# Optimization experiments

Measured on AMD Instinct MI355X. Metric: run time of the kernel, lower is better.

Reference implementation:

```python
import jax, jax.numpy as jnp
import numpy as np

N_N = 100000
N_E = 1600000
IN_DIM = 128
OUT_DIM = 128


def setup_inputs() -> dict:
    key = jax.random.key(0)
    k1, k2, k3, k4 = jax.random.split(key, 4)
    feats_n = jax.random.normal(k1, (N_N, IN_DIM), dtype=jnp.float32)
    # hs: guarantee every node appears at least once as a row (head) so degree > 0,
    # matching well-posed inputs for D**(-1/2) in the original module.
    hs = jnp.concatenate([
        jnp.arange(N_N, dtype=jnp.int64),
        jax.random.randint(k2, (N_E - N_N,), 0, N_N, dtype=jnp.int64),
    ])
    ts = jax.random.randint(k3, (N_E,), 0, N_N, dtype=jnp.int64)
    edges = jnp.stack([hs, ts], axis=0)  # [2, N_e]
    # Linear weight: normal(0,1) scaled by 1/sqrt(out_dim), no bias.
    weight = jax.random.normal(k4, (OUT_DIM, IN_DIM), dtype=jnp.float32) / np.sqrt(OUT_DIM)
    return {"feats_n": feats_n, "edges": edges, "weight": weight}


def reference(feats_n, edges, weight):
    hs, ts = edges[0], edges[1]
    n = feats_n.shape[0]
    # Degree = row-sum of adjacency (rows indexed by hs)
    deg = jax.ops.segment_sum(jnp.ones_like(hs, dtype=feats_n.dtype), hs, num_segments=n)
    sqrt_d_inv = deg ** (-0.5)  # [N_n]
    scaled = sqrt_d_inv[:, None] * feats_n  # [N_n, d]
    # SpMM: out[h] = sum over edges (h, t) of scaled[t]
    agg = jax.ops.segment_sum(scaled[ts], hs, num_segments=n)  # [N_n, d]
    msg = sqrt_d_inv[:, None] * agg
    out = msg @ weight.T  # Linear, no bias
    return jax.nn.relu(out)
```

## Files before the change

kernel.cpp:

```cpp
#include <hip/hip_runtime.h>

#define IN_DIM 128
#define CAP 64
#define NODE_SHIFT 8
#define BIN_NODES 256
#define NB_MAX 512
#define BCAP 5120
#define BINCAP_E 10240
#define CHUNK 4096

typedef __attribute__((ext_vector_type(8))) short bf16x8;
typedef __attribute__((ext_vector_type(4))) float f32x4;
typedef __attribute__((ext_vector_type(2))) float f32x2;

__device__ __forceinline__ unsigned short f2bf(float f) {
    unsigned int u = __float_as_uint(f);
    u += 0x7FFFu + ((u >> 16) & 1u);
    return (unsigned short)(u >> 16);
}

__global__ void k_prep(const float* __restrict__ W, bf16x8* __restrict__ Wsw,
                       int* __restrict__ bincur, int nbins,
                       unsigned int* __restrict__ dummy, float* __restrict__ rsd,
                       int n_n) {
    int gi = blockIdx.x * 256 + threadIdx.x;
    if (gi < nbins) bincur[gi] = 0;
    if (gi < 64) dummy[gi] = 0;
    if (gi == 64) rsd[n_n] = 0.0f;
    if (gi >= 2048) return;
    int n = gi >> 4, g = gi & 15;
    const float* wp = W + n * IN_DIM + g * 8;
    float4 a = *(const float4*)wp;
    float4 b = *(const float4*)(wp + 4);
    bf16x8 v;
    v[0] = (short)f2bf(a.x); v[1] = (short)f2bf(a.y);
    v[2] = (short)f2bf(a.z); v[3] = (short)f2bf(a.w);
    v[4] = (short)f2bf(b.x); v[5] = (short)f2bf(b.y);
    v[6] = (short)f2bf(b.z); v[7] = (short)f2bf(b.w);
    Wsw[n * 16 + (g ^ (n & 7))] = v;
}

__global__ __launch_bounds__(256) void k_partition(const int* __restrict__ edges, int n_e,
                                                   int nbins,
                                                   unsigned int* __restrict__ pairs,
                                                   int* __restrict__ bincur) {
    __shared__ unsigned long long sp[CHUNK];
    __shared__ int hist[NB_MAX];
    __shared__ int base[NB_MAX];
    int tid = threadIdx.x;
    int e0 = blockIdx.x * CHUNK;
    int nloc = n_e - e0;
    if (nloc > CHUNK) nloc = CHUNK;
    for (int i = tid; i < nbins; i += 256) hist[i] = 0;
    __syncthreads();
    for (int i = tid; i < nloc; i += 256) {
        int h = edges[e0 + i];
        int t = edges[n_e + e0 + i];
        sp[i] = ((unsigned long long)(unsigned int)h << 17) | (unsigned int)t;
        atomicAdd(&hist[h >> NODE_SHIFT], 1);
    }
    __syncthreads();
    for (int b = tid; b < nbins; b += 256) {
        int c = hist[b];
        base[b] = c ? atomicAdd(&bincur[b], c) : 0;
        hist[b] = 0;
    }
    __syncthreads();
    for (int i = tid; i < nloc; i += 256) {
        unsigned long long p = sp[i];
        int b = (int)(p >> (17 + NODE_SHIFT));
        int pos = atomicAdd(&hist[b], 1);
        int g = base[b] + pos;
        if (g < BCAP) pairs[(size_t)b * BCAP + g] = (unsigned int)(p & 0x1FFFFFFu);
    }
}

__global__ __launch_bounds__(256) void k_binmfma(const unsigned int* __restrict__ pairs,
                                                 const int* __restrict__ bincur,
                                                 int* __restrict__ bucket,
                                                 int2* __restrict__ rowinfo,
                                                 float* __restrict__ rsd,
                                                 const float* __restrict__ X,
                                                 const bf16x8* __restrict__ Wg,
                                                 unsigned short* __restrict__ Y2,
                                                 int n_n, int nbins) {
    __shared__ union {
        struct {
            unsigned int sp[BCAP];
            int lcur[BIN_NODES];
            int sbase[BIN_NODES];
            int wsum[4];
        } bs;
        bf16x8 wl[2048];
    } u;
    int tid = threadIdx.x;

    if ((int)blockIdx.x < nbins) {
        int b = blockIdx.x;
        u.bs.lcur[tid] = 0;
        __syncthreads();
        int n = bincur[b];
        if (n > BCAP) n = BCAP;
        const unsigned int* pp = pairs + (size_t)b * BCAP;
        for (int i = tid; i < n; i += 256) {
            unsigned int p = pp[i];
            u.bs.sp[i] = p;
            atomicAdd(&u.bs.lcur[p >> 17], 1);
        }
        __syncthreads();
        int draw = u.bs.lcur[tid];
        int dcap = draw < CAP ? draw : CAP;
        int v = (dcap + 15) & ~15;
        int lane = tid & 63, w = tid >> 6;
        int x = v;
        #pragma unroll
        for (int off = 1; off < 64; off <<= 1) {
            int y = __shfl_up(x, off);
            if (lane >= off) x += y;
        }
        if (lane == 63) u.bs.wsum[w] = x;
        __syncthreads();
        int wo = 0;
        for (int k = 0; k < w; ++k) wo += u.bs.wsum[k];
        int mybase = wo + x - v;
        u.bs.sbase[tid] = mybase;
        u.bs.lcur[tid] = 0;
        __syncthreads();
        int gbase = b * BINCAP_E;
        for (int i = tid; i < n; i += 256) {
            unsigned int p = u.bs.sp[i];
            int li = p >> 17;
            int t = p & 0x1FFFF;
            int pos = atomicAdd(&u.bs.lcur[li], 1);
            if (pos < CAP) {
                int idx = u.bs.sbase[li] + pos;
                if (idx < BINCAP_E) bucket[gbase + idx] = t;
            }
        }
        __syncthreads();
        int h = (b << NODE_SHIFT) + tid;
        if (h < n_n) {
            for (int s = dcap; s < v; ++s) {
                int idx = mybase + s;
                if (idx < BINCAP_E) bucket[gbase + idx] = n_n;
            }
            rowinfo[h] = make_int2(gbase + mybase, dcap);
            rsd[h] = draw > 0 ? rsqrtf((float)draw) : 0.0f;
        }
    } else {
        int M = n_n;
        int mb = blockIdx.x - nbins;
        for (int i = tid; i < 2048; i += 256) u.wl[i] = Wg[i];
        __syncthreads();
        int slab = mb * 4 + (tid >> 6);
        int m0 = slab * 16;
        if (m0 >= M) return;
        int l = tid & 63;
        int lm = l & 15, lk = l >> 4;
        int row = m0 + lm;
        int rowc = row < M ? row : M - 1;
        bf16x8 xf[4];
        const float* xbase = X + (size_t)rowc * IN_DIM + lk * 8;
        #pragma unroll
        for (int ks = 0; ks < 4; ++ks) {
            float4 a = *(const float4*)(xbase + ks * 32);
            float4 b2 = *(const float4*)(xbase + ks * 32 + 4);
            bf16x8 v;
            v[0] = (short)f2bf(a.x); v[1] = (short)f2bf(a.y);
            v[2] = (short)f2bf(a.z); v[3] = (short)f2bf(a.w);
            v[4] = (short)f2bf(b2.x); v[5] = (short)f2bf(b2.y);
            v[6] = (short)f2bf(b2.z); v[7] = (short)f2bf(b2.w);
            xf[ks] = v;
        }
        #pragma unroll
        for (int nt = 0; nt < 8; ++nt) {
            f32x4 acc = {0.f, 0.f, 0.f, 0.f};
            #pragma unroll
            for (int ks = 0; ks < 4; ++ks) {
                int nn = nt * 16 + lm;
                int g = ks * 4 + lk;
                bf16x8 wf = u.wl[nn * 16 + (g ^ (nn & 7))];
                acc = __builtin_amdgcn_mfma_f32_16x16x32_bf16(wf, xf[ks], acc, 0, 0, 0);
            }
            if (row < M) {
                unsigned int lo = (unsigned int)f2bf(acc[0]) |
                                  ((unsigned int)f2bf(acc[1]) << 16);
                unsigned int hi = (unsigned int)f2bf(acc[2]) |
                                  ((unsigned int)f2bf(acc[3]) << 16);
                uint2* yp = (uint2*)(Y2 + (size_t)row * IN_DIM + nt * 16 + lk * 4);
                *yp = make_uint2(lo, hi);
            }
        }
    }
}

__global__ __launch_bounds__(256) void k_agg(const uint4* __restrict__ Y4,
                                             const int* __restrict__ bucket,
                                             const int2* __restrict__ rowinfo,
                                             const float* __restrict__ rsd,
                                             float* __restrict__ out, int n_n) {
    int gw = (int)((blockIdx.x * 256u + threadIdx.x) >> 6);
    int lane = threadIdx.x & 63;
    if (gw >= n_n) return;
    int2 ri = rowinfo[gw];
    int d = ri.y;
    int nb = (d + 15) >> 4;
    const uint4* bk4 = (const uint4*)(bucket + ri.x);
    int grp = lane >> 4, a = lane & 15;
    f32x2 a0 = {0.f, 0.f}, a1 = {0.f, 0.f}, a2 = {0.f, 0.f}, a3 = {0.f, 0.f};

    uint4 tv = bk4[grp];
    for (int b = 0; b < nb; ++b) {
        int bn = (b + 1 < nb) ? b + 1 : b;
        uint4 tvn = bk4[bn * 4 + grp];
        float s0 = rsd[tv.x], s1 = rsd[tv.y], s2 = rsd[tv.z], s3 = rsd[tv.w];
        uint4 v0 = Y4[(size_t)tv.x * 16 + a];
        uint4 v1 = Y4[(size_t)tv.y * 16 + a];
        uint4 v2 = Y4[(size_t)tv.z * 16 + a];
        uint4 v3 = Y4[(size_t)tv.w * 16 + a];
        #define ACCUM(V, S)                                                   \
        {                                                                     \
            f32x2 sv; sv[0] = (S); sv[1] = (S);                               \
            f32x2 x;                                                          \
            x[0] = __uint_as_float((V).x << 16);                              \
            x[1] = __uint_as_float((V).x & 0xffff0000u);                      \
            asm("v_pk_fma_f32 %0, %1, %2, %0" : "+v"(a0) : "v"(x), "v"(sv));  \
            x[0] = __uint_as_float((V).y << 16);                              \
            x[1] = __uint_as_float((V).y & 0xffff0000u);                      \
            asm("v_pk_fma_f32 %0, %1, %2, %0" : "+v"(a1) : "v"(x), "v"(sv));  \
            x[0] = __uint_as_float((V).z << 16);                              \
            x[1] = __uint_as_float((V).z & 0xffff0000u);                      \
            asm("v_pk_fma_f32 %0, %1, %2, %0" : "+v"(a2) : "v"(x), "v"(sv));  \
            x[0] = __uint_as_float((V).w << 16);                              \
            x[1] = __uint_as_float((V).w & 0xffff0000u);                      \
            asm("v_pk_fma_f32 %0, %1, %2, %0" : "+v"(a3) : "v"(x), "v"(sv));  \
        }
        ACCUM(v0, s0) ACCUM(v1, s1) ACCUM(v2, s2) ACCUM(v3, s3)
        #undef ACCUM
        tv = tvn;
    }
    #define MERGE(A)                                                          \
    {                                                                         \
        A[0] += __shfl_xor(A[0], 16); A[1] += __shfl_xor(A[1], 16);           \
        A[0] += __shfl_xor(A[0], 32); A[1] += __shfl_xor(A[1], 32);           \
    }
    MERGE(a0) MERGE(a1) MERGE(a2) MERGE(a3)
    #undef MERGE
    if (lane < 16) {
        float s = rsd[gw];
        float4 o0 = make_float4(fmaxf(a0[0] * s, 0.f), fmaxf(a0[1] * s, 0.f),
                                fmaxf(a1[0] * s, 0.f), fmaxf(a1[1] * s, 0.f));
        float4 o1 = make_float4(fmaxf(a2[0] * s, 0.f), fmaxf(a2[1] * s, 0.f),
                                fmaxf(a3[0] * s, 0.f), fmaxf(a3[1] * s, 0.f));
        float4* op = (float4*)(out + (size_t)gw * IN_DIM + a * 8);
        op[0] = o0;
        op[1] = o1;
    }
}

extern "C" void kernel_launch(void* const* d_in, const int* in_sizes, int n_in,
                              void* d_out, int out_size, void* d_ws, size_t ws_size,
                              hipStream_t stream) {
    const float* X = (const float*)d_in[0];
    const int* edges = (const int*)d_in[1];
    const float* W = (const float*)d_in[2];
    int n_n = in_sizes[0] / IN_DIM;
    int n_e = in_sizes[1] / 2;
    int nbins = (n_n + BIN_NODES - 1) >> NODE_SHIFT;

    char* ws = (char*)d_ws;
    size_t o = 0;
    auto take = [&](size_t bytes) -> char* {
        char* p = ws + o;
        o += (bytes + 511) & ~(size_t)511;
        return p;
    };
    float* rsd = (float*)take((size_t)(n_n + 1) * 4);
    int2* rowinfo = (int2*)take((size_t)n_n * 8);
    int* bucket = (int*)take((size_t)nbins * BINCAP_E * 4);
    unsigned short* Y2 = (unsigned short*)take((size_t)(n_n + 1) * IN_DIM * 2);
    unsigned int* pairs = (unsigned int*)take((size_t)nbins * BCAP * 4);
    int* bincur = (int*)take((size_t)nbins * 4);
    bf16x8* Wsw = (bf16x8*)take(2048 * 16);

    int nslab = (n_n + 15) / 16;
    int nmf = (nslab + 3) / 4;
    k_prep<<<8, 256, 0, stream>>>(W, Wsw, bincur, nbins,
                                  (unsigned int*)(Y2 + (size_t)n_n * IN_DIM), rsd, n_n);
    k_partition<<<(n_e + CHUNK - 1) / CHUNK, 256, 0, stream>>>(edges, n_e, nbins, pairs, bincur);
    k_binmfma<<<nbins + nmf, 256, 0, stream>>>(pairs, bincur, bucket, rowinfo, rsd,
                                               X, Wsw, Y2, n_n, nbins);
    k_agg<<<(n_n + 3) / 4, 256, 0, stream>>>((const uint4*)Y2, bucket, rowinfo, rsd,
                                             (float*)d_out, n_n);
}
```

Before: 119.2 us.

## Co-schedule dense GEMM with edge partition instead of bin scatter

Moves the X·W^T bf16 MFMA blocks out of the bin-scatter kernel and into the edge-partition kernel, which is then split into a fused partition+GEMM launch and a standalone bin-scatter launch. The dense GEMM now overlaps the atomic-heavy edge partition, while the bin-scatter runs alone afterward. This rebalances work across kernels, but the partition blocks now share an LDS union sized for the larger 32KB sp array, which may reduce occupancy of the GEMM blocks.

```diff
diff --git a/kernel.cpp b/kernel.cpp
--- a/kernel.cpp
+++ b/kernel.cpp
@@ -40,116 +40,53 @@
     Wsw[n * 16 + (g ^ (n & 7))] = v;
 }
 
-__global__ __launch_bounds__(256) void k_partition(const int* __restrict__ edges, int n_e,
-                                                   int nbins,
-                                                   unsigned int* __restrict__ pairs,
-                                                   int* __restrict__ bincur) {
-    __shared__ unsigned long long sp[CHUNK];
-    __shared__ int hist[NB_MAX];
-    __shared__ int base[NB_MAX];
-    int tid = threadIdx.x;
-    int e0 = blockIdx.x * CHUNK;
-    int nloc = n_e - e0;
-    if (nloc > CHUNK) nloc = CHUNK;
-    for (int i = tid; i < nbins; i += 256) hist[i] = 0;
-    __syncthreads();
-    for (int i = tid; i < nloc; i += 256) {
-        int h = edges[e0 + i];
-        int t = edges[n_e + e0 + i];
-        sp[i] = ((unsigned long long)(unsigned int)h << 17) | (unsigned int)t;
-        atomicAdd(&hist[h >> NODE_SHIFT], 1);
-    }
-    __syncthreads();
-    for (int b = tid; b < nbins; b += 256) {
-        int c = hist[b];
-        base[b] = c ? atomicAdd(&bincur[b], c) : 0;
-        hist[b] = 0;
-    }
-    __syncthreads();
-    for (int i = tid; i < nloc; i += 256) {
-        unsigned long long p = sp[i];
-        int b = (int)(p >> (17 + NODE_SHIFT));
-        int pos = atomicAdd(&hist[b], 1);
-        int g = base[b] + pos;
-        if (g < BCAP) pairs[(size_t)b * BCAP + g] = (unsigned int)(p & 0x1FFFFFFu);
-    }
-}
-
-__global__ __launch_bounds__(256) void k_binmfma(const unsigned int* __restrict__ pairs,
-                                                 const int* __restrict__ bincur,
-                                                 int* __restrict__ bucket,
-                                                 int2* __restrict__ rowinfo,
-                                                 float* __restrict__ rsd,
-                                                 const float* __restrict__ X,
-                                                 const bf16x8* __restrict__ Wg,
-                                                 unsigned short* __restrict__ Y2,
-                                                 int n_n, int nbins) {
+__global__ __launch_bounds__(256) void k_partgemm(const int* __restrict__ edges, int n_e,
+                                                  int nbins, int npart,
+                                                  unsigned int* __restrict__ pairs,
+                                                  int* __restrict__ bincur,
+                                                  const float* __restrict__ X,
+                                                  const bf16x8* __restrict__ Wg,
+                                                  unsigned short* __restrict__ Y2,
+                                                  int n_n) {
     __shared__ union {
         struct {
-            unsigned int sp[BCAP];
-            int lcur[BIN_NODES];
-            int sbase[BIN_NODES];
-            int wsum[4];
-        } bs;
+            unsigned long long sp[CHUNK];
+            int hist[NB_MAX];
+            int base[NB_MAX];
+        } pt;
         bf16x8 wl[2048];
     } u;
     int tid = threadIdx.x;
 
-    if ((int)blockIdx.x < nbins) {
-        int b = blockIdx.x;
-        u.bs.lcur[tid] = 0;
-        __syncthreads();
-        int n = bincur[b];
-        if (n > BCAP) n = BCAP;
-        const unsigned int* pp = pairs + (size_t)b * BCAP;
-        for (int i = tid; i < n; i += 256) {
-            unsigned int p = pp[i];
-            u.bs.sp[i] = p;
-            atomicAdd(&u.bs.lcur[p >> 17], 1);
-        }
-        __syncthreads();
-        int draw = u.bs.lcur[tid];
-        int dcap = draw < CAP ? draw : CAP;
-        int v = (dcap + 15) & ~15;
-        int lane = tid & 63, w = tid >> 6;
-        int x = v;
-        #pragma unroll
-        for (int off = 1; off < 64; off <<= 1) {
-            int y = __shfl_up(x, off);
-            if (lane >= off) x += y;
-        }
-        if (lane == 63) u.bs.wsum[w] = x;
-        __syncthreads();
-        int wo = 0;
-        for (int k = 0; k < w; ++k) wo += u.bs.wsum[k];
-        int mybase = wo + x - v;
-        u.bs.sbase[tid] = mybase;
-        u.bs.lcur[tid] = 0;
-        __syncthreads();
-        int gbase = b * BINCAP_E;
-        for (int i = tid; i < n; i += 256) {
-            unsigned int p = u.bs.sp[i];
-            int li = p >> 17;
-            int t = p & 0x1FFFF;
-            int pos = atomicAdd(&u.bs.lcur[li], 1);
-            if (pos < CAP) {
-                int idx = u.bs.sbase[li] + pos;
-                if (idx < BINCAP_E) bucket[gbase + idx] = t;
-            }
-        }
-        __syncthreads();
-        int h = (b << NODE_SHIFT) + tid;
-        if (h < n_n) {
-            for (int s = dcap; s < v; ++s) {
-                int idx = mybase + s;
-                if (idx < BINCAP_E) bucket[gbase + idx] = n_n;
-            }
-            rowinfo[h] = make_int2(gbase + mybase, dcap);
-            rsd[h] = draw > 0 ? rsqrtf((float)draw) : 0.0f;
+    if ((int)blockIdx.x < npart) {
+        int e0 = blockIdx.x * CHUNK;
+        int nloc = n_e - e0;
+        if (nloc > CHUNK) nloc = CHUNK;
+        for (int i = tid; i < nbins; i += 256) u.pt.hist[i] = 0;
+        __syncthreads();
+        for (int i = tid; i < nloc; i += 256) {
+            int h = edges[e0 + i];
+            int t = edges[n_e + e0 + i];
+            u.pt.sp[i] = ((unsigned long long)(unsigned int)h << 17) | (unsigned int)t;
+            atomicAdd(&u.pt.hist[h >> NODE_SHIFT], 1);
+        }
+        __syncthreads();
+        for (int b = tid; b < nbins; b += 256) {
+            int c = u.pt.hist[b];
+            u.pt.base[b] = c ? atomicAdd(&bincur[b], c) : 0;
+            u.pt.hist[b] = 0;
+        }
+        __syncthreads();
+        for (int i = tid; i < nloc; i += 256) {
+            unsigned long long p = u.pt.sp[i];
+            int b = (int)(p >> (17 + NODE_SHIFT));
+            int pos = atomicAdd(&u.pt.hist[b], 1);
+            int g = u.pt.base[b] + pos;
+            if (g < BCAP) pairs[(size_t)b * BCAP + g] = (unsigned int)(p & 0x1FFFFFFu);
         }
     } else {
         int M = n_n;
-        int mb = blockIdx.x - nbins;
+        int mb = blockIdx.x - npart;
         for (int i = tid; i < 2048; i += 256) u.wl[i] = Wg[i];
         __syncthreads();
         int slab = mb * 4 + (tid >> 6);
@@ -191,6 +128,69 @@
                 *yp = make_uint2(lo, hi);
             }
         }
+    }
+}
+
+__global__ __launch_bounds__(256) void k_binscatter(const unsigned int* __restrict__ pairs,
+                                                    const int* __restrict__ bincur,
+                                                    int* __restrict__ bucket,
+                                                    int2* __restrict__ rowinfo,
+                                                    float* __restrict__ rsd, int n_n) {
+    __shared__ unsigned int sp[BCAP];
+    __shared__ int lcur[BIN_NODES];
+    __shared__ int sbase[BIN_NODES];
+    __shared__ int wsum[4];
+    int b = blockIdx.x;
+    int tid = threadIdx.x;
+    lcur[tid] = 0;
+    __syncthreads();
+    int n = bincur[b];
+    if (n > BCAP) n = BCAP;
+    const unsigned int* pp = pairs + (size_t)b * BCAP;
+    for (int i = tid; i < n; i += 256) {
+        unsigned int p = pp[i];
+        sp[i] = p;
+        atomicAdd(&lcur[p >> 17], 1);
+    }
+    __syncthreads();
+    int draw = lcur[tid];
+    int dcap = draw < CAP ? draw : CAP;
+    int v = (dcap + 15) & ~15;
+    int lane = tid & 63, w = tid >> 6;
+    int x = v;
+    #pragma unroll
+    for (int off = 1; off < 64; off <<= 1) {
+        int y = __shfl_up(x, off);
+        if (lane >= off) x += y;
+    }
+    if (lane == 63) wsum[w] = x;
+    __syncthreads();
+    int wo = 0;
+    for (int k = 0; k < w; ++k) wo += wsum[k];
+    int mybase = wo + x - v;
+    sbase[tid] = mybase;
+    lcur[tid] = 0;
+    __syncthreads();
+    int gbase = b * BINCAP_E;
+    for (int i = tid; i < n; i += 256) {
+        unsigned int p = sp[i];
+        int li = p >> 17;
+        int t = p & 0x1FFFF;
+        int pos = atomicAdd(&lcur[li], 1);
+        if (pos < CAP) {
+            int idx = sbase[li] + pos;
+            if (idx < BINCAP_E) bucket[gbase + idx] = t;
+        }
+    }
+    __syncthreads();
+    int h = (b << NODE_SHIFT) + tid;
+    if (h < n_n) {
+        for (int s = dcap; s < v; ++s) {
+            int idx = mybase + s;
+            if (idx < BINCAP_E) bucket[gbase + idx] = n_n;
+        }
+        rowinfo[h] = make_int2(gbase + mybase, dcap);
+        rsd[h] = draw > 0 ? rsqrtf((float)draw) : 0.0f;
     }
 }
 
@@ -285,11 +285,12 @@
 
     int nslab = (n_n + 15) / 16;
     int nmf = (nslab + 3) / 4;
+    int npart = (n_e + CHUNK - 1) / CHUNK;
     k_prep<<<8, 256, 0, stream>>>(W, Wsw, bincur, nbins,
                                   (unsigned int*)(Y2 + (size_t)n_n * IN_DIM), rsd, n_n);
-    k_partition<<<(n_e + CHUNK - 1) / CHUNK, 256, 0, stream>>>(edges, n_e, nbins, pairs, bincur);
-    k_binmfma<<<nbins + nmf, 256, 0, stream>>>(pairs, bincur, bucket, rowinfo, rsd,
-                                               X, Wsw, Y2, n_n, nbins);
+    k_partgemm<<<npart + nmf, 256, 0, stream>>>(edges, n_e, nbins, npart, pairs, bincur,
+                                                X, Wsw, Y2, n_n);
+    k_binscatter<<<nbins, 256, 0, stream>>>(pairs, bincur, bucket, rowinfo, rsd, n_n);
     k_agg<<<(n_n + 3) / 4, 256, 0, stream>>>((const uint4*)Y2, bucket, rowinfo, rsd,
                                              (float*)d_out, n_n);
 }
```

New measurement: 119.3 us. About the same (+0.1%).

## Split dense GEMM blocks across partition and binning kernels, pack pairs in 32 bits

Applied to the files above, without the earlier changes.

Moves about four fifths of the X·W^T MFMA blocks into the edge-partition kernel so they run alongside partitioning, and keeps the rest in the binning kernel. The partition stage now reads edges with int4 vector loads and stores 32-bit packed (local head, tail) pairs in shared memory instead of 64-bit ones, re-reading the head indices for the scatter pass. The aim is to fill idle compute units during the atomic-heavy partition phase and to cut shared-memory and load traffic. In exchange the partition kernel's shared-memory footprint is set by the union with the weight tile, which can affect occupancy, and the int4 loads assume 16-byte aligned chunk offsets.

```diff
diff --git a/kernel.cpp b/kernel.cpp
--- a/kernel.cpp
+++ b/kernel.cpp
@@ -40,38 +40,124 @@
     Wsw[n * 16 + (g ^ (n & 7))] = v;
 }
 
-__global__ __launch_bounds__(256) void k_partition(const int* __restrict__ edges, int n_e,
-                                                   int nbins,
-                                                   unsigned int* __restrict__ pairs,
-                                                   int* __restrict__ bincur) {
-    __shared__ unsigned long long sp[CHUNK];
-    __shared__ int hist[NB_MAX];
-    __shared__ int base[NB_MAX];
+__device__ __forceinline__ void gemm_role(bf16x8* wl, const float* __restrict__ X,
+                                          const bf16x8* __restrict__ Wg,
+                                          unsigned short* __restrict__ Y2,
+                                          int M, int mb, int tid) {
+    for (int i = tid; i < 2048; i += 256) wl[i] = Wg[i];
+    __syncthreads();
+    int slab = mb * 4 + (tid >> 6);
+    int m0 = slab * 16;
+    if (m0 >= M) return;
+    int l = tid & 63;
+    int lm = l & 15, lk = l >> 4;
+    int row = m0 + lm;
+    int rowc = row < M ? row : M - 1;
+    bf16x8 xf[4];
+    const float* xbase = X + (size_t)rowc * IN_DIM + lk * 8;
+    #pragma unroll
+    for (int ks = 0; ks < 4; ++ks) {
+        float4 a = *(const float4*)(xbase + ks * 32);
+        float4 b2 = *(const float4*)(xbase + ks * 32 + 4);
+        bf16x8 v;
+        v[0] = (short)f2bf(a.x); v[1] = (short)f2bf(a.y);
+        v[2] = (short)f2bf(a.z); v[3] = (short)f2bf(a.w);
+        v[4] = (short)f2bf(b2.x); v[5] = (short)f2bf(b2.y);
+        v[6] = (short)f2bf(b2.z); v[7] = (short)f2bf(b2.w);
+        xf[ks] = v;
+    }
+    #pragma unroll
+    for (int nt = 0; nt < 8; ++nt) {
+        f32x4 acc = {0.f, 0.f, 0.f, 0.f};
+        #pragma unroll
+        for (int ks = 0; ks < 4; ++ks) {
+            int nn = nt * 16 + lm;
+            int g = ks * 4 + lk;
+            bf16x8 wf = wl[nn * 16 + (g ^ (nn & 7))];
+            acc = __builtin_amdgcn_mfma_f32_16x16x32_bf16(wf, xf[ks], acc, 0, 0, 0);
+        }
+        if (row < M) {
+            unsigned int lo = (unsigned int)f2bf(acc[0]) |
+                              ((unsigned int)f2bf(acc[1]) << 16);
+            unsigned int hi = (unsigned int)f2bf(acc[2]) |
+                              ((unsigned int)f2bf(acc[3]) << 16);
+            uint2* yp = (uint2*)(Y2 + (size_t)row * IN_DIM + nt * 16 + lk * 4);
+            *yp = make_uint2(lo, hi);
+        }
+    }
+}
+
+__global__ __launch_bounds__(256) void k_partgemm(const int* __restrict__ edges, int n_e,
+                                                  int nbins, int npart,
+                                                  unsigned int* __restrict__ pairs,
+                                                  int* __restrict__ bincur,
+                                                  const float* __restrict__ X,
+                                                  const bf16x8* __restrict__ Wg,
+                                                  unsigned short* __restrict__ Y2,
+                                                  int n_n) {
+    __shared__ union {
+        struct {
+            unsigned int sp[CHUNK];
+            int hist[NB_MAX];
+            int base[NB_MAX];
+        } pt;
+        bf16x8 wl[2048];
+    } u;
     int tid = threadIdx.x;
-    int e0 = blockIdx.x * CHUNK;
-    int nloc = n_e - e0;
-    if (nloc > CHUNK) nloc = CHUNK;
-    for (int i = tid; i < nbins; i += 256) hist[i] = 0;
-    __syncthreads();
-    for (int i = tid; i < nloc; i += 256) {
-        int h = edges[e0 + i];
-        int t = edges[n_e + e0 + i];
-        sp[i] = ((unsigned long long)(unsigned int)h << 17) | (unsigned int)t;
-        atomicAdd(&hist[h >> NODE_SHIFT], 1);
-    }
-    __syncthreads();
-    for (int b = tid; b < nbins; b += 256) {
-        int c = hist[b];
-        base[b] = c ? atomicAdd(&bincur[b], c) : 0;
-        hist[b] = 0;
-    }
-    __syncthreads();
-    for (int i = tid; i < nloc; i += 256) {
-        unsigned long long p = sp[i];
-        int b = (int)(p >> (17 + NODE_SHIFT));
-        int pos = atomicAdd(&hist[b], 1);
-        int g = base[b] + pos;
-        if (g < BCAP) pairs[(size_t)b * BCAP + g] = (unsigned int)(p & 0x1FFFFFFu);
+
+    if ((int)blockIdx.x < npart) {
+        int e0 = blockIdx.x * CHUNK;
+        int nloc = n_e - e0;
+        if (nloc > CHUNK) nloc = CHUNK;
+        int nloc4 = nloc >> 2;
+        const int* hsrc = edges + e0;
+        const int* tsrc = edges + n_e + e0;
+        for (int i = tid; i < nbins; i += 256) u.pt.hist[i] = 0;
+        __syncthreads();
+        for (int j = tid; j < nloc4; j += 256) {
+            int4 hv = ((const int4*)hsrc)[j];
+            int4 tv = ((const int4*)tsrc)[j];
+            u.pt.sp[4 * j + 0] = ((unsigned int)(hv.x & 255) << 17) | (unsigned int)tv.x;
+            u.pt.sp[4 * j + 1] = ((unsigned int)(hv.y & 255) << 17) | (unsigned int)tv.y;
+            u.pt.sp[4 * j + 2] = ((unsigned int)(hv.z & 255) << 17) | (unsigned int)tv.z;
+            u.pt.sp[4 * j + 3] = ((unsigned int)(hv.w & 255) << 17) | (unsigned int)tv.w;
+            atomicAdd(&u.pt.hist[hv.x >> NODE_SHIFT], 1);
+            atomicAdd(&u.pt.hist[hv.y >> NODE_SHIFT], 1);
+            atomicAdd(&u.pt.hist[hv.z >> NODE_SHIFT], 1);
+            atomicAdd(&u.pt.hist[hv.w >> NODE_SHIFT], 1);
+        }
+        for (int i = (nloc4 << 2) + tid; i < nloc; i += 256) {
+            int h = hsrc[i];
+            u.pt.sp[i] = ((unsigned int)(h & 255) << 17) | (unsigned int)tsrc[i];
+            atomicAdd(&u.pt.hist[h >> NODE_SHIFT], 1);
+        }
+        __syncthreads();
+        for (int b = tid; b < nbins; b += 256) {
+            int c = u.pt.hist[b];
+            u.pt.base[b] = c ? atomicAdd(&bincur[b], c) : 0;
+            u.pt.hist[b] = 0;
+        }
+        __syncthreads();
+        for (int j = tid; j < nloc4; j += 256) {
+            int4 hv = ((const int4*)hsrc)[j];
+            int bs[4] = {hv.x >> NODE_SHIFT, hv.y >> NODE_SHIFT,
+                         hv.z >> NODE_SHIFT, hv.w >> NODE_SHIFT};
+            #pragma unroll
+            for (int k = 0; k < 4; ++k) {
+                int b = bs[k];
+                int pos = atomicAdd(&u.pt.hist[b], 1);
+                int g = u.pt.base[b] + pos;
+                if (g < BCAP) pairs[(size_t)b * BCAP + g] = u.pt.sp[4 * j + k];
+            }
+        }
+        for (int i = (nloc4 << 2) + tid; i < nloc; i += 256) {
+            int b = hsrc[i] >> NODE_SHIFT;
+            int pos = atomicAdd(&u.pt.hist[b], 1);
+            int g = u.pt.base[b] + pos;
+            if (g < BCAP) pairs[(size_t)b * BCAP + g] = u.pt.sp[i];
+        }
+    } else {
+        gemm_role(u.wl, X, Wg, Y2, n_n, blockIdx.x - npart, tid);
     }
 }
 
@@ -83,7 +169,7 @@
                                                  const float* __restrict__ X,
                                                  const bf16x8* __restrict__ Wg,
                                                  unsigned short* __restrict__ Y2,
-                                                 int n_n, int nbins) {
+                                                 int n_n, int nbins, int mb0) {
     __shared__ union {
         struct {
             unsigned int sp[BCAP];
@@ -148,49 +234,7 @@
             rsd[h] = draw > 0 ? rsqrtf((float)draw) : 0.0f;
         }
     } else {
-        int M = n_n;
-        int mb = blockIdx.x - nbins;
-        for (int i = tid; i < 2048; i += 256) u.wl[i] = Wg[i];
-        __syncthreads();
-        int slab = mb * 4 + (tid >> 6);
-        int m0 = slab * 16;
-        if (m0 >= M) return;
-        int l = tid & 63;
-        int lm = l & 15, lk = l >> 4;
-        int row = m0 + lm;
-        int rowc = row < M ? row : M - 1;
-        bf16x8 xf[4];
-        const float* xbase = X + (size_t)rowc * IN_DIM + lk * 8;
-        #pragma unroll
-        for (int ks = 0; ks < 4; ++ks) {
-            float4 a = *(const float4*)(xbase + ks * 32);
-            float4 b2 = *(const float4*)(xbase + ks * 32 + 4);
-            bf16x8 v;
-            v[0] = (short)f2bf(a.x); v[1] = (short)f2bf(a.y);
-            v[2] = (short)f2bf(a.z); v[3] = (short)f2bf(a.w);
-            v[4] = (short)f2bf(b2.x); v[5] = (short)f2bf(b2.y);
-            v[6] = (short)f2bf(b2.z); v[7] = (short)f2bf(b2.w);
-            xf[ks] = v;
-        }
-        #pragma unroll
-        for (int nt = 0; nt < 8; ++nt) {
-            f32x4 acc = {0.f, 0.f, 0.f, 0.f};
-            #pragma unroll
-            for (int ks = 0; ks < 4; ++ks) {
-                int nn = nt * 16 + lm;
-                int g = ks * 4 + lk;
-                bf16x8 wf = u.wl[nn * 16 + (g ^ (nn & 7))];
-                acc = __builtin_amdgcn_mfma_f32_16x16x32_bf16(wf, xf[ks], acc, 0, 0, 0);
-            }
-            if (row < M) {
-                unsigned int lo = (unsigned int)f2bf(acc[0]) |
-                                  ((unsigned int)f2bf(acc[1]) << 16);
-                unsigned int hi = (unsigned int)f2bf(acc[2]) |
-                                  ((unsigned int)f2bf(acc[3]) << 16);
-                uint2* yp = (uint2*)(Y2 + (size_t)row * IN_DIM + nt * 16 + lk * 4);
-                *yp = make_uint2(lo, hi);
-            }
-        }
+        gemm_role(u.wl, X, Wg, Y2, n_n, blockIdx.x - nbins + mb0, tid);
     }
 }
 
@@ -285,11 +329,15 @@
 
     int nslab = (n_n + 15) / 16;
     int nmf = (nslab + 3) / 4;
+    int nmf1 = (nmf * 4) / 5;
+    int nmf2 = nmf - nmf1;
+    int npart = (n_e + CHUNK - 1) / CHUNK;
     k_prep<<<8, 256, 0, stream>>>(W, Wsw, bincur, nbins,
                                   (unsigned int*)(Y2 + (size_t)n_n * IN_DIM), rsd, n_n);
-    k_partition<<<(n_e + CHUNK - 1) / CHUNK, 256, 0, stream>>>(edges, n_e, nbins, pairs, bincur);
-    k_binmfma<<<nbins + nmf, 256, 0, stream>>>(pairs, bincur, bucket, rowinfo, rsd,
-                                               X, Wsw, Y2, n_n, nbins);
+    k_partgemm<<<npart + nmf1, 256, 0, stream>>>(edges, n_e, nbins, npart, pairs, bincur,
+                                                 X, Wsw, Y2, n_n);
+    k_binmfma<<<nbins + nmf2, 256, 0, stream>>>(pairs, bincur, bucket, rowinfo, rsd,
+                                                X, Wsw, Y2, n_n, nbins, nmf1);
     k_agg<<<(n_n + 3) / 4, 256, 0, stream>>>((const uint4*)Y2, bucket, rowinfo, rsd,
                                              (float*)d_out, n_n);
 }
```

Measured after the change: 118.5 us. About the same (-0.6%).

## Fuse prep, partition and bin/MFMA kernels into one launch with counter handoff

Applied to the files above, without the earlier changes.

Merges the weight-prep, edge-partition and bin/MFMA kernels into a single launch. Partition blocks signal a global done counter, and bin blocks spin on it before reading pairs. Partitioning now reads head and tail indices as int4 vectors, reading the heads twice instead of staging them in shared memory. CHUNK is doubled, and each MFMA block converts W to bf16 itself instead of using a precomputed copy. This removes two launch boundaries and lets the feature GEMM overlap partitioning, at the cost of redundant W conversion, a spin-wait that relies on block scheduling order, and no longer zeroing the Y2 padding row.

```diff
diff --git a/kernel.cpp b/kernel.cpp
--- a/kernel.cpp
+++ b/kernel.cpp
@@ -7,7 +7,7 @@
 #define NB_MAX 512
 #define BCAP 5120
 #define BINCAP_E 10240
-#define CHUNK 4096
+#define CHUNK 8192
 
 typedef __attribute__((ext_vector_type(8))) short bf16x8;
 typedef __attribute__((ext_vector_type(4))) float f32x4;
@@ -19,139 +19,93 @@
     return (unsigned short)(u >> 16);
 }
 
-__global__ void k_prep(const float* __restrict__ W, bf16x8* __restrict__ Wsw,
-                       int* __restrict__ bincur, int nbins,
-                       unsigned int* __restrict__ dummy, float* __restrict__ rsd,
-                       int n_n) {
-    int gi = blockIdx.x * 256 + threadIdx.x;
-    if (gi < nbins) bincur[gi] = 0;
-    if (gi < 64) dummy[gi] = 0;
-    if (gi == 64) rsd[n_n] = 0.0f;
-    if (gi >= 2048) return;
-    int n = gi >> 4, g = gi & 15;
-    const float* wp = W + n * IN_DIM + g * 8;
-    float4 a = *(const float4*)wp;
-    float4 b = *(const float4*)(wp + 4);
-    bf16x8 v;
-    v[0] = (short)f2bf(a.x); v[1] = (short)f2bf(a.y);
-    v[2] = (short)f2bf(a.z); v[3] = (short)f2bf(a.w);
-    v[4] = (short)f2bf(b.x); v[5] = (short)f2bf(b.y);
-    v[6] = (short)f2bf(b.z); v[7] = (short)f2bf(b.w);
-    Wsw[n * 16 + (g ^ (n & 7))] = v;
-}
-
-__global__ __launch_bounds__(256) void k_partition(const int* __restrict__ edges, int n_e,
-                                                   int nbins,
-                                                   unsigned int* __restrict__ pairs,
-                                                   int* __restrict__ bincur) {
-    __shared__ unsigned long long sp[CHUNK];
-    __shared__ int hist[NB_MAX];
-    __shared__ int base[NB_MAX];
-    int tid = threadIdx.x;
-    int e0 = blockIdx.x * CHUNK;
-    int nloc = n_e - e0;
-    if (nloc > CHUNK) nloc = CHUNK;
-    for (int i = tid; i < nbins; i += 256) hist[i] = 0;
-    __syncthreads();
-    for (int i = tid; i < nloc; i += 256) {
-        int h = edges[e0 + i];
-        int t = edges[n_e + e0 + i];
-        sp[i] = ((unsigned long long)(unsigned int)h << 17) | (unsigned int)t;
-        atomicAdd(&hist[h >> NODE_SHIFT], 1);
-    }
-    __syncthreads();
-    for (int b = tid; b < nbins; b += 256) {
-        int c = hist[b];
-        base[b] = c ? atomicAdd(&bincur[b], c) : 0;
-        hist[b] = 0;
-    }
-    __syncthreads();
-    for (int i = tid; i < nloc; i += 256) {
-        unsigned long long p = sp[i];
-        int b = (int)(p >> (17 + NODE_SHIFT));
-        int pos = atomicAdd(&hist[b], 1);
-        int g = base[b] + pos;
-        if (g < BCAP) pairs[(size_t)b * BCAP + g] = (unsigned int)(p & 0x1FFFFFFu);
-    }
-}
-
-__global__ __launch_bounds__(256) void k_binmfma(const unsigned int* __restrict__ pairs,
-                                                 const int* __restrict__ bincur,
-                                                 int* __restrict__ bucket,
-                                                 int2* __restrict__ rowinfo,
-                                                 float* __restrict__ rsd,
-                                                 const float* __restrict__ X,
-                                                 const bf16x8* __restrict__ Wg,
-                                                 unsigned short* __restrict__ Y2,
-                                                 int n_n, int nbins) {
+__global__ __launch_bounds__(256) void k_fused(const int* __restrict__ edges, int n_e,
+                                               int nbins, int npart, int nmf,
+                                               unsigned int* __restrict__ pairs,
+                                               int* __restrict__ bincur,
+                                               int* __restrict__ done,
+                                               int* __restrict__ bucket,
+                                               int2* __restrict__ rowinfo,
+                                               float* __restrict__ rsd,
+                                               const float* __restrict__ X,
+                                               const float* __restrict__ W,
+                                               unsigned short* __restrict__ Y2,
+                                               int n_n) {
     __shared__ union {
-        struct {
-            unsigned int sp[BCAP];
-            int lcur[BIN_NODES];
-            int sbase[BIN_NODES];
-            int wsum[4];
-        } bs;
+        struct { int hist[NB_MAX]; int base[NB_MAX]; } pt;
+        struct { unsigned int sp[BCAP]; int lcur[BIN_NODES];
+                 int sbase[BIN_NODES]; int wsum[4]; } bs;
         bf16x8 wl[2048];
     } u;
     int tid = threadIdx.x;
-
-    if ((int)blockIdx.x < nbins) {
-        int b = blockIdx.x;
-        u.bs.lcur[tid] = 0;
-        __syncthreads();
-        int n = bincur[b];
-        if (n > BCAP) n = BCAP;
-        const unsigned int* pp = pairs + (size_t)b * BCAP;
-        for (int i = tid; i < n; i += 256) {
-            unsigned int p = pp[i];
-            u.bs.sp[i] = p;
-            atomicAdd(&u.bs.lcur[p >> 17], 1);
-        }
-        __syncthreads();
-        int draw = u.bs.lcur[tid];
-        int dcap = draw < CAP ? draw : CAP;
-        int v = (dcap + 15) & ~15;
-        int lane = tid & 63, w = tid >> 6;
-        int x = v;
+    int bid = blockIdx.x;
+
+    if (bid < npart) {
+        int e0 = bid * CHUNK;
+        int nloc = n_e - e0;
+        if (nloc > CHUNK) nloc = CHUNK;
+        int nloc4 = nloc >> 2;
+        const int* hsrc = edges + e0;
+        const int* tsrc = edges + n_e + e0;
+        for (int i = tid; i < nbins; i += 256) u.pt.hist[i] = 0;
+        __syncthreads();
+        for (int j = tid; j < nloc4; j += 256) {
+            int4 hv = ((const int4*)hsrc)[j];
+            atomicAdd(&u.pt.hist[hv.x >> NODE_SHIFT], 1);
+            atomicAdd(&u.pt.hist[hv.y >> NODE_SHIFT], 1);
+            atomicAdd(&u.pt.hist[hv.z >> NODE_SHIFT], 1);
+            atomicAdd(&u.pt.hist[hv.w >> NODE_SHIFT], 1);
+        }
+        for (int i = (nloc4 << 2) + tid; i < nloc; i += 256)
+            atomicAdd(&u.pt.hist[hsrc[i] >> NODE_SHIFT], 1);
+        __syncthreads();
+        for (int b = tid; b < nbins; b += 256) {
+            int c = u.pt.hist[b];
+            u.pt.base[b] = c ? atomicAdd(&bincur[b], c) : 0;
+            u.pt.hist[b] = 0;
+        }
+        __syncthreads();
+        for (int j = tid; j < nloc4; j += 256) {
+            int4 hv = ((const int4*)hsrc)[j];
+            int4 tv = ((const int4*)tsrc)[j];
+            #define PUT(H, T)                                                 \
+            {                                                                 \
+                int b = (H) >> NODE_SHIFT;                                    \
+                int pos = atomicAdd(&u.pt.hist[b], 1);                        \
+                int g = u.pt.base[b] + pos;                                   \
+                if (g < BCAP)                                                 \
+                    pairs[(size_t)b * BCAP + g] =                             \
+                        ((unsigned int)((H) & 255) << 17) | (unsigned int)(T);\
+            }
+            PUT(hv.x, tv.x) PUT(hv.y, tv.y) PUT(hv.z, tv.z) PUT(hv.w, tv.w)
+        }
+        for (int i = (nloc4 << 2) + tid; i < nloc; i += 256) {
+            int h = hsrc[i], t = tsrc[i];
+            PUT(h, t)
+        }
+        #undef PUT
+        __threadfence();
+        __syncthreads();
+        if (tid == 0)
+            __hip_atomic_fetch_add(done, 1, __ATOMIC_RELEASE, __HIP_MEMORY_SCOPE_AGENT);
+    } else if (bid < npart + nmf) {
+        int mb = bid - npart;
         #pragma unroll
-        for (int off = 1; off < 64; off <<= 1) {
-            int y = __shfl_up(x, off);
-            if (lane >= off) x += y;
-        }
-        if (lane == 63) u.bs.wsum[w] = x;
-        __syncthreads();
-        int wo = 0;
-        for (int k = 0; k < w; ++k) wo += u.bs.wsum[k];
-        int mybase = wo + x - v;
-        u.bs.sbase[tid] = mybase;
-        u.bs.lcur[tid] = 0;
-        __syncthreads();
-        int gbase = b * BINCAP_E;
-        for (int i = tid; i < n; i += 256) {
-            unsigned int p = u.bs.sp[i];
-            int li = p >> 17;
-            int t = p & 0x1FFFF;
-            int pos = atomicAdd(&u.bs.lcur[li], 1);
-            if (pos < CAP) {
-                int idx = u.bs.sbase[li] + pos;
-                if (idx < BINCAP_E) bucket[gbase + idx] = t;
-            }
-        }
-        __syncthreads();
-        int h = (b << NODE_SHIFT) + tid;
-        if (h < n_n) {
-            for (int s = dcap; s < v; ++s) {
-                int idx = mybase + s;
-                if (idx < BINCAP_E) bucket[gbase + idx] = n_n;
-            }
-            rowinfo[h] = make_int2(gbase + mybase, dcap);
-            rsd[h] = draw > 0 ? rsqrtf((float)draw) : 0.0f;
-        }
-    } else {
+        for (int k = 0; k < 8; ++k) {
+            int gi = tid + k * 256;
+            int n = gi >> 4, g = gi & 15;
+            const float* wp = W + n * IN_DIM + g * 8;
+            float4 a = *(const float4*)wp;
+            float4 b2 = *(const float4*)(wp + 4);
+            bf16x8 v;
+            v[0] = (short)f2bf(a.x); v[1] = (short)f2bf(a.y);
+            v[2] = (short)f2bf(a.z); v[3] = (short)f2bf(a.w);
+            v[4] = (short)f2bf(b2.x); v[5] = (short)f2bf(b2.y);
+            v[6] = (short)f2bf(b2.z); v[7] = (short)f2bf(b2.w);
+            u.wl[n * 16 + (g ^ (n & 7))] = v;
+        }
+        __syncthreads();
         int M = n_n;
-        int mb = blockIdx.x - nbins;
-        for (int i = tid; i < 2048; i += 256) u.wl[i] = Wg[i];
-        __syncthreads();
         int slab = mb * 4 + (tid >> 6);
         int m0 = slab * 16;
         if (m0 >= M) return;
@@ -190,6 +144,66 @@
                 uint2* yp = (uint2*)(Y2 + (size_t)row * IN_DIM + nt * 16 + lk * 4);
                 *yp = make_uint2(lo, hi);
             }
+        }
+    } else {
+        int b = bid - npart - nmf;
+        if (tid == 0) {
+            while (__hip_atomic_load(done, __ATOMIC_ACQUIRE, __HIP_MEMORY_SCOPE_AGENT) < npart)
+                __builtin_amdgcn_s_sleep(16);
+        }
+        __syncthreads();
+        __threadfence();
+        u.bs.lcur[tid] = 0;
+        __syncthreads();
+        int n = bincur[b];
+        if (n > BCAP) n = BCAP;
+        const unsigned int* pp = pairs + (size_t)b * BCAP;
+        for (int i = tid; i < n; i += 256) {
+            unsigned int p = pp[i];
+            u.bs.sp[i] = p;
+            atomicAdd(&u.bs.lcur[p >> 17], 1);
+        }
+        __syncthreads();
+        int draw = u.bs.lcur[tid];
+        int dcap = draw < CAP ? draw : CAP;
+        int v = (dcap + 15) & ~15;
+        int lane = tid & 63, w = tid >> 6;
+        int x = v;
+        #pragma unroll
+        for (int off = 1; off < 64; off <<= 1) {
+            int y = __shfl_up(x, off);
+            if (lane >= off) x += y;
+        }
+        if (lane == 63) u.bs.wsum[w] = x;
+        __syncthreads();
+        int wo = 0;
+        for (int k = 0; k < w; ++k) wo += u.bs.wsum[k];
+        int mybase = wo + x - v;
+        u.bs.sbase[tid] = mybase;
+        u.bs.lcur[tid] = 0;
+        __syncthreads();
+        int gbase = b * BINCAP_E;
+        for (int i = tid; i < n; i += 256) {
+            unsigned int p = u.bs.sp[i];
+            int li = p >> 17;
+            int t = p & 0x1FFFF;
+            int pos = atomicAdd(&u.bs.lcur[li], 1);
+            if (pos < CAP) {
+                int idx = u.bs.sbase[li] + pos;
+                if (idx < BINCAP_E) bucket[gbase + idx] = t;
+            }
+        }
+        __syncthreads();
+        int h = (b << NODE_SHIFT) + tid;
+        if (h < n_n) {
+            for (int s = dcap; s < v; ++s) {
+                int idx = mybase + s;
+                if (idx < BINCAP_E) bucket[gbase + idx] = n_n;
+            }
+            rowinfo[h] = make_int2(gbase + mybase, dcap);
+            rsd[h] = draw > 0 ? rsqrtf((float)draw) : 0.0f;
+        } else if (h == n_n) {
+            rsd[n_n] = 0.0f;
         }
     }
 }
@@ -280,16 +294,16 @@
     int* bucket = (int*)take((size_t)nbins * BINCAP_E * 4);
     unsigned short* Y2 = (unsigned short*)take((size_t)(n_n + 1) * IN_DIM * 2);
     unsigned int* pairs = (unsigned int*)take((size_t)nbins * BCAP * 4);
-    int* bincur = (int*)take((size_t)nbins * 4);
-    bf16x8* Wsw = (bf16x8*)take(2048 * 16);
+    int* bincur = (int*)take((size_t)(nbins + 1) * 4);
+    int* done = bincur + nbins;
 
     int nslab = (n_n + 15) / 16;
     int nmf = (nslab + 3) / 4;
-    k_prep<<<8, 256, 0, stream>>>(W, Wsw, bincur, nbins,
-                                  (unsigned int*)(Y2 + (size_t)n_n * IN_DIM), rsd, n_n);
-    k_partition<<<(n_e + CHUNK - 1) / CHUNK, 256, 0, stream>>>(edges, n_e, nbins, pairs, bincur);
-    k_binmfma<<<nbins + nmf, 256, 0, stream>>>(pairs, bincur, bucket, rowinfo, rsd,
-                                               X, Wsw, Y2, n_n, nbins);
+    int npart = (n_e + CHUNK - 1) / CHUNK;
+    hipMemsetAsync(bincur, 0, (size_t)(nbins + 1) * 4, stream);
+    k_fused<<<npart + nmf + nbins, 256, 0, stream>>>(edges, n_e, nbins, npart, nmf,
+                                                     pairs, bincur, done, bucket,
+                                                     rowinfo, rsd, X, W, Y2, n_n);
     k_agg<<<(n_n + 3) / 4, 256, 0, stream>>>((const uint4*)Y2, bucket, rowinfo, rsd,
                                              (float*)d_out, n_n);
 }
```

New measurement: 272.5 us. 129% more time.
